# Optimization experiments

Measured on AMD Instinct MI355X. Metric: run time of the kernel, lower is better.

The kernel has to match this reference:

```python
import jax, jax.numpy as jnp
import numpy as np

BETA = 15.0  # soft-max temperature used by the common Erosion2d/Dilation2d (soft_max=True)
EPS = 1e-5


def _morph(x, w, dilation, kind):
    """Channel-wise soft morphological op over a KxK dilated window ('same' padding).
    erosion: -logsumexp(beta*(w - patch))/beta ; dilation: logsumexp(beta*(w + patch))/beta.
    """
    B, C, H, W = x.shape
    K = w.shape[-1]
    eff = K + (K - 1) * (dilation - 1)
    pb = (eff - 1) // 2
    pe = (eff - 1) - pb
    xp = jnp.pad(x, ((0, 0), (0, 0), (pb, pe), (pb, pe)))
    taps = [xp[:, :, i * dilation:i * dilation + H, j * dilation:j * dilation + W]
            for i in range(K) for j in range(K)]
    patches = jnp.stack(taps, axis=2)                      # (B, C, K*K, H, W)
    wf = w.reshape(C, K * K, 1, 1)                          # broadcast over B, H, W
    z = (wf - patches) if kind == 'erosion' else (wf + patches)
    out = jax.scipy.special.logsumexp(z * BETA, axis=2) / BETA  # (B, C, H, W)
    return -out if kind == 'erosion' else out


def _bn(x, gamma, beta):
    """BatchNorm2d in training mode: batch statistics over (B, H, W) per channel."""
    mean = jnp.mean(x, axis=(0, 2, 3), keepdims=True)
    var = jnp.var(x, axis=(0, 2, 3), keepdims=True)
    g = gamma.reshape(1, -1, 1, 1)
    b = beta.reshape(1, -1, 1, 1)
    return g * (x - mean) * jax.lax.rsqrt(var + EPS) + b


def setup_inputs() -> dict:
    key = jax.random.key(0)
    ks = jax.random.split(key, 5)
    B, C, H, W, K = 8, 64, 192, 192, 3
    x = jax.random.normal(ks[0], (B, C, H, W), jnp.float32)
    # morphology structuring elements (torch init is zeros; small randn for a nontrivial test)
    we = jax.random.normal(ks[1], (3, C, K, K), jnp.float32) * 0.1
    wd = jax.random.normal(ks[2], (3, C, K, K), jnp.float32) * 0.1
    # per-branch BN affine params (torch default: gamma=1, beta=0)
    bn_ge = jnp.ones((3, C), jnp.float32)
    bn_be = jnp.zeros((3, C), jnp.float32)
    bn_gd = jnp.ones((3, C), jnp.float32)
    bn_bd = jnp.zeros((3, C), jnp.float32)
    # 1x1 conv (3C -> 1, no bias): weight (1, 3C, 1, 1) stored flat as (3C,)
    conve_w = jax.random.normal(ks[3], (3 * C,), jnp.float32) * 0.05
    convd_w = jax.random.normal(ks[4], (3 * C,), jnp.float32) * 0.05
    g_e = jnp.ones((1,), jnp.float32)
    b_e = jnp.zeros((1,), jnp.float32)
    g_d = jnp.ones((1,), jnp.float32)
    b_d = jnp.zeros((1,), jnp.float32)
    return dict(x=x, we=we, wd=wd, bn_ge=bn_ge, bn_be=bn_be, bn_gd=bn_gd, bn_bd=bn_bd,
                conve_w=conve_w, convd_w=convd_w, g_e=g_e, b_e=b_e, g_d=g_d, b_d=b_d)


def reference(x, we, wd, bn_ge, bn_be, bn_gd, bn_bd, conve_w, convd_w, g_e, b_e, g_d, b_d):
    # three erosion branches (dilations 1,2,3), each followed by its own BN
    xe = jnp.concatenate([
        _bn(_morph(x, we[i], i + 1, 'erosion'), bn_ge[i], bn_be[i]) for i in range(3)
    ], axis=1)                                              # (B, 3C, H, W)
    xd = jnp.concatenate([
        _bn(_morph(x, wd[i], i + 1, 'dilation'), bn_gd[i], bn_bd[i]) for i in range(3)
    ], axis=1)
    # 1x1 conv to 1 channel + BN + ReLU
    ye = jnp.einsum('bchw,c->bhw', xe, conve_w)[:, None]    # (B, 1, H, W)
    ye = jax.nn.relu(_bn(ye, g_e, b_e))
    yd = jnp.einsum('bchw,c->bhw', xd, convd_w)[:, None]
    yd = jax.nn.relu(_bn(yd, g_d, b_d))
    return jnp.concatenate([ye, yd], axis=1)                # (B, 2, H, W)
```

## Files before the change

### kernel.cpp

```cpp
#include <hip/hip_runtime.h>


#define BETA 15.0f
#define MSHIFT 25.0f
#define INV_BETA (1.0f/15.0f)
#define LN2 0.6931471805599453f
#define EPSB 1e-5f
#define Hn 192
#define Wn 192
#define HWn (192*192)
#define N1 (8*192*192)
#define SFLOOR 1e-37f

#define STDH 70
#define STDW 70
#define STSTR 72
#define SNPAIR (STDH*35)

#define RDH 38
#define RSTR 40
#define RNPAIR (RDH*19)
#define RPITER 3

#define WS_SUM   0
#define WS_SQS   384
#define WS_SCAL  768
#define WS_WG    772
#define WS_YE    (772 + 3456)
#define WS_YD    (WS_YE + 294912)
#define WS_SLAB  (WS_YE + 2*294912)

__global__ void k_wexp(const float* __restrict__ we,
                       const float* __restrict__ wd,
                       float* __restrict__ ws) {
    int idx = blockIdx.x * 256 + threadIdx.x;
    if (idx < 772) ws[idx] = 0.f;
    if (idx >= 3456) return;
    int kb = idx / 576;
    int rem = idx - kb * 576;
    float w = (kb < 3) ? we[kb * 576 + rem] : wd[(kb - 3) * 576 + rem];
    ws[WS_WG + idx] = __expf(BETA * w);
}

template<int D, int H, int STR>
__device__ __forceinline__ void sweepT(const float* __restrict__ P,
                                       int py0, int px,
                                       const float* __restrict__ wgp,
                                       float* __restrict__ S) {
    float W[9];
#pragma unroll
    for (int k2 = 0; k2 < 9; ++k2) W[k2] = wgp[k2];
#pragma unroll
    for (int k = 0; k < H; ++k) S[k] = 0.f;
    const float* base = P + (py0 - D + 3) * STR + (px - D);
#pragma unroll
    for (int r = 0; r < H + 2 * D; ++r) {
        float va = base[r * STR];
        float vb = base[r * STR + D];
        float vc = base[r * STR + 2 * D];
#pragma unroll
        for (int i = 0; i < 3; ++i) {
            int k = r - i * D;
            if (k >= 0 && k < H) {
                S[k] = fmaf(W[i*3+0], va, S[k]);
                S[k] = fmaf(W[i*3+1], vb, S[k]);
                S[k] = fmaf(W[i*3+2], vc, S[k]);
            }
        }
    }
}

template<int D>
__device__ __forceinline__ void sweep2(const float* __restrict__ P,
                                       int py0, int tcol,
                                       const float* __restrict__ wgp,
                                       float* __restrict__ SA,
                                       float* __restrict__ SB) {
    float W[9];
#pragma unroll
    for (int k2 = 0; k2 < 9; ++k2) W[k2] = wgp[k2];
#pragma unroll
    for (int k = 0; k < 8; ++k) { SA[k] = 0.f; SB[k] = 0.f; }
    const int colbase = (D == 1) ? (2 * tcol + 2) : (2 * tcol);
#pragma unroll
    for (int r = 0; r < 8 + 2 * D; ++r) {
        const float2* row =
            (const float2*)(P + (py0 - D + 3 + r) * STSTR + colbase);
        float2 v0 = row[0], v1 = row[1];
        float ta0, ta1, ta2, tb0, tb1, tb2;
        if (D == 1) {
            ta0 = v0.x; ta1 = v0.y; ta2 = v1.x;
            tb0 = v0.y; tb1 = v1.x; tb2 = v1.y;
        } else {
            float2 v2 = row[2], v3 = row[3];
            if (D == 2) {
                ta0 = v0.y; ta1 = v1.y; ta2 = v2.y;
                tb0 = v1.x; tb1 = v2.x; tb2 = v3.x;
            } else {
                ta0 = v0.x; ta1 = v1.y; ta2 = v3.x;
                tb0 = v0.y; tb1 = v2.x; tb2 = v3.y;
            }
        }
#pragma unroll
        for (int i = 0; i < 3; ++i) {
            int k = r - i * D;
            if (k >= 0 && k < 8) {
                SA[k] = fmaf(W[i*3+0], ta0, SA[k]);
                SA[k] = fmaf(W[i*3+1], ta1, SA[k]);
                SA[k] = fmaf(W[i*3+2], ta2, SA[k]);
                SB[k] = fmaf(W[i*3+0], tb0, SB[k]);
                SB[k] = fmaf(W[i*3+1], tb1, SB[k]);
                SB[k] = fmaf(W[i*3+2], tb2, SB[k]);
            }
        }
    }
}

__device__ __forceinline__ void red2(float a, float b2, int lane, float* rs, float* rq) {
#pragma unroll
    for (int off = 32; off; off >>= 1) {
        a  += __shfl_down(a, off, 64);
        b2 += __shfl_down(b2, off, 64);
    }
    if (lane == 0) { *rs = a; *rq = b2; }
}

__global__ __launch_bounds__(256, 3) void k_stats(
    const float* __restrict__ x, const float* __restrict__ wg,
    float* __restrict__ sum, float* __restrict__ sqs) {
    __shared__ float EX[STDH * STSTR], EY[STDH * STSTR];
    __shared__ float redS[4][6], redQ[4][6];
    const int tid = threadIdx.x;
    const int p = blockIdx.y;
    const int c = p & 63;
    const int t = blockIdx.x;
    const int h0 = (t / 3) * 64, w0 = (t % 3) * 64;

    const float* xp = x + (size_t)p * HWn;
    {
        int r = tid / 35, pp = tid - r * 35;
        for (int l = tid; l < SNPAIR; l += 256) {
            int gh = h0 - 3 + r;
            int gw0 = w0 - 3 + 2 * pp;
            float va = 0.f, vb = 0.f;
            if ((unsigned)gh < (unsigned)Hn) {
                if ((unsigned)gw0 < (unsigned)Wn)       va = xp[gh * Wn + gw0];
                if ((unsigned)(gw0+1) < (unsigned)Wn)   vb = xp[gh * Wn + gw0 + 1];
            }
            float ba = BETA * va, bb = BETA * vb;
            *(float2*)&EX[r * STSTR + 2 * pp] =
                make_float2(__expf(-ba - MSHIFT), __expf(-bb - MSHIFT));
            *(float2*)&EY[r * STSTR + 2 * pp] =
                make_float2(__expf( ba - MSHIFT), __expf( bb - MSHIFT));
            r += 7; pp += 11;
            if (pp >= 35) { pp -= 35; ++r; }
        }
    }
    __syncthreads();

    const int tcol = tid & 31;
    const int py0 = (tid >> 5) * 8;
    const int lane = tid & 63, wv = tid >> 6;
    const float LI = LN2 * INV_BETA, MI = MSHIFT * INV_BETA;

#define DO_BR_STATS(D, SLOT, PL, AL, AM) { \
    float SA[8], SB[8]; \
    sweep2<D>(PL, py0, tcol, wg + (SLOT) * 576 + c * 9, SA, SB); \
    float sv = 0.f, qv = 0.f; \
    _Pragma("unroll") \
    for (int k = 0; k < 8; ++k) { \
        float ma = fmaf(__log2f(fmaxf(SA[k], SFLOOR)), AL, AM); \
        float mb = fmaf(__log2f(fmaxf(SB[k], SFLOOR)), AL, AM); \
        sv += ma + mb; qv = fmaf(ma, ma, fmaf(mb, mb, qv)); \
    } \
    red2(sv, qv, lane, &redS[wv][SLOT], &redQ[wv][SLOT]); }

    DO_BR_STATS(1, 0, EX, -LI, -MI)
    DO_BR_STATS(2, 1, EX, -LI, -MI)
    DO_BR_STATS(3, 2, EX, -LI, -MI)
    DO_BR_STATS(1, 3, EY,  LI,  MI)
    DO_BR_STATS(2, 4, EY,  LI,  MI)
    DO_BR_STATS(3, 5, EY,  LI,  MI)
#undef DO_BR_STATS

    __syncthreads();
    if (tid < 6)
        atomicAdd(&sum[tid * 64 + c],
                  redS[0][tid] + redS[1][tid] + redS[2][tid] + redS[3][tid]);
    else if (tid < 12) {
        int v = tid - 6;
        atomicAdd(&sqs[v * 64 + c],
                  redQ[0][v] + redQ[1][v] + redQ[2][v] + redQ[3][v]);
    }
}

__device__ __forceinline__ void alpha_fill(
    const float* __restrict__ sum, const float* __restrict__ sqs,
    const float* __restrict__ bn_ge, const float* __restrict__ bn_gd,
    const float* __restrict__ conve, const float* __restrict__ convd,
    float* __restrict__ al, int tid) {
    for (int l = tid; l < 384; l += 256) {
        int side_ = l / 192, ch = l - side_ * 192;
        float mean = sum[l] * (1.0f / N1);
        float var  = sqs[l] * (1.0f / N1) - mean * mean;
        float inv  = rsqrtf(fmaxf(var, 0.f) + EPSB);
        float g  = side_ ? bn_gd[ch] : bn_ge[ch];
        float cw = side_ ? convd[ch] : conve[ch];
        float sgn = side_ ? 1.f : -1.f;
        al[l] = sgn * cw * g * inv * INV_BETA * LN2;
    }
}

template<int NS>
__global__ __launch_bounds__(256, 4) void k_reduce(
    const float* __restrict__ x, const float* __restrict__ wg,
    const float* __restrict__ sum, const float* __restrict__ sqs,
    const float* __restrict__ bn_ge, const float* __restrict__ bn_gd,
    const float* __restrict__ conve, const float* __restrict__ convd,
    float* __restrict__ ye, float* __restrict__ yd,
    float* __restrict__ slab, float* __restrict__ scal) {
    constexpr int NC = 64 / NS;
    __shared__ float EX[RDH * RSTR], EY[RDH * RSTR];
    __shared__ float al[384];
    __shared__ float redA[4][4];
    const int tid = threadIdx.x;
    const int t = blockIdx.x;
    const int b = blockIdx.y;
    const int grp = blockIdx.z;
    const int c0 = grp * NC;
    const int tr = t / 6, tc = t - tr * 6;
    const int h0 = tr * 32, w0 = tc * 32;
    const int px = (tid & 31) + 3;
    const int py0 = (tid >> 5) * 4;
    const float* xb = x + (size_t)b * 64 * HWn;

    alpha_fill(sum, sqs, bn_ge, bn_gd, conve, convd, al, tid);

    float accE[4] = {0.f, 0.f, 0.f, 0.f}, accD[4] = {0.f, 0.f, 0.f, 0.f};
    float2 L[RPITER];

    {
        const float* xp = xb + (size_t)c0 * HWn;
        int r = tid / 19, pp = tid - r * 19;
#pragma unroll
        for (int i = 0; i < RPITER; ++i) {
            int l = tid + i * 256;
            float va = 0.f, vb = 0.f;
            if (l < RNPAIR) {
                int gh = h0 - 3 + r, gw0 = w0 - 3 + 2 * pp;
                if ((unsigned)gh < (unsigned)Hn) {
                    if ((unsigned)gw0 < (unsigned)Wn)     va = xp[gh * Wn + gw0];
                    if ((unsigned)(gw0+1) < (unsigned)Wn) vb = xp[gh * Wn + gw0 + 1];
                }
            }
            L[i] = make_float2(va, vb);
            r += 13; pp += 9;
            if (pp >= 19) { pp -= 19; ++r; }
        }
    }

    for (int ci = 0; ci < NC; ++ci) {
        __syncthreads();
        {
            int r = tid / 19, pp = tid - r * 19;
#pragma unroll
            for (int i = 0; i < RPITER; ++i) {
                int l = tid + i * 256;
                if (l < RNPAIR) {
                    float ba = BETA * L[i].x, bb = BETA * L[i].y;
                    *(float2*)&EX[r * RSTR + 2 * pp] =
                        make_float2(__expf(-ba - MSHIFT), __expf(-bb - MSHIFT));
                    *(float2*)&EY[r * RSTR + 2 * pp] =
                        make_float2(__expf( ba - MSHIFT), __expf( bb - MSHIFT));
                }
                r += 13; pp += 9;
                if (pp >= 19) { pp -= 19; ++r; }
            }
        }
        __syncthreads();
        if (ci < NC - 1) {
            const float* xp = xb + (size_t)(c0 + ci + 1) * HWn;
            int r = tid / 19, pp = tid - r * 19;
#pragma unroll
            for (int i = 0; i < RPITER; ++i) {
                int l = tid + i * 256;
                float va = 0.f, vb = 0.f;
                if (l < RNPAIR) {
                    int gh = h0 - 3 + r, gw0 = w0 - 3 + 2 * pp;
                    if ((unsigned)gh < (unsigned)Hn) {
                        if ((unsigned)gw0 < (unsigned)Wn)     va = xp[gh * Wn + gw0];
                        if ((unsigned)(gw0+1) < (unsigned)Wn) vb = xp[gh * Wn + gw0 + 1];
                    }
                }
                L[i] = make_float2(va, vb);
                r += 13; pp += 9;
                if (pp >= 19) { pp -= 19; ++r; }
            }
        }
        const int c = c0 + ci;
#define DO_BR_ACC(D, SIDE, BR, PL, ACC) { \
        float S[4]; \
        sweepT<D, 4, RSTR>(PL, py0, px, wg + ((SIDE) * 3 + (BR)) * 576 + c * 9, S); \
        const float a_ = al[(SIDE) * 192 + (BR) * 64 + c]; \
        _Pragma("unroll") \
        for (int k = 0; k < 4; ++k) \
            ACC[k] = fmaf(a_, __log2f(fmaxf(S[k], SFLOOR)), ACC[k]); }

        DO_BR_ACC(1, 0, 0, EX, accE)
        DO_BR_ACC(2, 0, 1, EX, accE)
        DO_BR_ACC(3, 0, 2, EX, accE)
        DO_BR_ACC(1, 1, 0, EY, accD)
        DO_BR_ACC(2, 1, 1, EY, accD)
        DO_BR_ACC(3, 1, 2, EY, accD)
#undef DO_BR_ACC
    }

    if constexpr (NS == 1) {
        const int oidx = b * HWn + (h0 + py0) * Wn + (w0 + px - 3);
#pragma unroll
        for (int k = 0; k < 4; ++k) {
            ye[oidx + k * Wn] = accE[k];
            yd[oidx + k * Wn] = accD[k];
        }
        float se = 0.f, qe = 0.f, sd = 0.f, qd = 0.f;
#pragma unroll
        for (int k = 0; k < 4; ++k) {
            se += accE[k]; qe = fmaf(accE[k], accE[k], qe);
            sd += accD[k]; qd = fmaf(accD[k], accD[k], qd);
        }
        const int lane = tid & 63, wv = tid >> 6;
        float v4[4] = {se, qe, sd, qd};
#pragma unroll
        for (int j = 0; j < 4; ++j) {
            float tv = v4[j];
#pragma unroll
            for (int off = 32; off; off >>= 1) tv += __shfl_down(tv, off, 64);
            if (lane == 0) redA[wv][j] = tv;
        }
        __syncthreads();
        if (tid < 4)
            atomicAdd(&scal[tid],
                      redA[0][tid] + redA[1][tid] + redA[2][tid] + redA[3][tid]);
    } else {
        float* pe = slab + ((size_t)grp * 8 + b) * HWn;
        float* pd = slab + ((size_t)(NS + grp) * 8 + b) * HWn;
        const int oidx = (h0 + py0) * Wn + (w0 + px - 3);
#pragma unroll
        for (int k = 0; k < 4; ++k) {
            pe[oidx + k * Wn] = accE[k];
            pd[oidx + k * Wn] = accD[k];
        }
    }
}

template<int NS>
__global__ __launch_bounds__(256) void k_fsum(
    const float* __restrict__ slab,
    float* __restrict__ ye, float* __restrict__ yd, float* __restrict__ scal) {
    int i = blockIdx.x * 256 + threadIdx.x;
    int b = i / HWn, rem = i - b * HWn;
    float e = 0.f, d = 0.f;
#pragma unroll
    for (int g = 0; g < NS; ++g) {
        e += slab[((size_t)g * 8 + b) * HWn + rem];
        d += slab[((size_t)(NS + g) * 8 + b) * HWn + rem];
    }
    ye[i] = e; yd[i] = d;
    float v[4] = {e, e * e, d, d * d};
    __shared__ float red[4][4];
    int lane = threadIdx.x & 63, wv = threadIdx.x >> 6;
#pragma unroll
    for (int k = 0; k < 4; ++k) {
        float tv = v[k];
#pragma unroll
        for (int off = 32; off; off >>= 1) tv += __shfl_down(tv, off, 64);
        if (lane == 0) red[wv][k] = tv;
    }
    __syncthreads();
    if (threadIdx.x < 4)
        atomicAdd(&scal[threadIdx.x],
                  red[0][threadIdx.x] + red[1][threadIdx.x] + red[2][threadIdx.x] + red[3][threadIdx.x]);
}

__global__ __launch_bounds__(256) void k_final(
    const float* __restrict__ ye, const float* __restrict__ yd,
    const float* __restrict__ scal,
    const float* __restrict__ g_e, const float* __restrict__ b_e,
    const float* __restrict__ g_d, const float* __restrict__ b_d,
    float* __restrict__ out) {
    int i = blockIdx.x * 256 + threadIdx.x;
    float me_ = scal[0] * (1.0f / N1);
    float ve  = scal[1] * (1.0f / N1) - me_ * me_;
    float ie  = rsqrtf(fmaxf(ve, 0.f) + EPSB);
    float md_ = scal[2] * (1.0f / N1);
    float vd  = scal[3] * (1.0f / N1) - md_ * md_;
    float idv = rsqrtf(fmaxf(vd, 0.f) + EPSB);
    float ge = g_e[0], be = b_e[0];
    float gd = g_d[0], bd = b_d[0];
    int b = i / HWn, rem = i - b * HWn;
    float oe = fmaxf(ge * (ye[i] - me_) * ie + be, 0.f);
    float od = fmaxf(gd * (yd[i] - md_) * idv + bd, 0.f);
    out[(size_t)(b * 2) * HWn + rem]     = oe;
    out[(size_t)(b * 2 + 1) * HWn + rem] = od;
}

extern "C" void kernel_launch(void* const* d_in, const int* in_sizes, int n_in,
                              void* d_out, int out_size, void* d_ws, size_t ws_size,
                              hipStream_t stream) {
    const float* x     = (const float*)d_in[0];
    const float* we    = (const float*)d_in[1];
    const float* wd    = (const float*)d_in[2];
    const float* bn_ge = (const float*)d_in[3];
    const float* bn_gd = (const float*)d_in[5];
    const float* conve = (const float*)d_in[7];
    const float* convd = (const float*)d_in[8];
    const float* g_e   = (const float*)d_in[9];
    const float* b_e   = (const float*)d_in[10];
    const float* g_d   = (const float*)d_in[11];
    const float* b_d   = (const float*)d_in[12];
    float* ws = (float*)d_ws;

    const size_t need4 = (size_t)(WS_SLAB + 4 * 2 * 294912) * sizeof(float);
    const size_t need2 = (size_t)(WS_SLAB + 2 * 2 * 294912) * sizeof(float);
    const int ns = (ws_size >= need4) ? 4 : (ws_size >= need2) ? 2 : 1;

    hipLaunchKernelGGL(k_wexp, dim3(14), dim3(256), 0, stream, we, wd, ws);
    hipLaunchKernelGGL(k_stats, dim3(9, 512), dim3(256), 0, stream,
                       x, ws + WS_WG, ws + WS_SUM, ws + WS_SQS);
    if (ns == 4) {
        hipLaunchKernelGGL((k_reduce<4>), dim3(36, 8, 4), dim3(256), 0, stream,
                           x, ws + WS_WG, ws + WS_SUM, ws + WS_SQS, bn_ge, bn_gd,
                           conve, convd, ws + WS_YE, ws + WS_YD, ws + WS_SLAB,
                           ws + WS_SCAL);
        hipLaunchKernelGGL((k_fsum<4>), dim3(1152), dim3(256), 0, stream,
                           ws + WS_SLAB, ws + WS_YE, ws + WS_YD, ws + WS_SCAL);
    } else if (ns == 2) {
        hipLaunchKernelGGL((k_reduce<2>), dim3(36, 8, 2), dim3(256), 0, stream,
                           x, ws + WS_WG, ws + WS_SUM, ws + WS_SQS, bn_ge, bn_gd,
                           conve, convd, ws + WS_YE, ws + WS_YD, ws + WS_SLAB,
                           ws + WS_SCAL);
        hipLaunchKernelGGL((k_fsum<2>), dim3(1152), dim3(256), 0, stream,
                           ws + WS_SLAB, ws + WS_YE, ws + WS_YD, ws + WS_SCAL);
    } else {
        hipLaunchKernelGGL((k_reduce<1>), dim3(36, 8, 1), dim3(256), 0, stream,
                           x, ws + WS_WG, ws + WS_SUM, ws + WS_SQS, bn_ge, bn_gd,
                           conve, convd, ws + WS_YE, ws + WS_YD, ws, ws + WS_SCAL);
    }
    hipLaunchKernelGGL(k_final, dim3(1152), dim3(256), 0, stream,
                       ws + WS_YE, ws + WS_YD, ws + WS_SCAL, g_e, b_e, g_d, b_d,
                       (float*)d_out);
}
```

Before: 282.0 us.

## Drop weight-exp kernel, replace stats atomics with partials, stop materializing ye/yd

```diff
diff --git a/kernel.cpp b/kernel.cpp
--- a/kernel.cpp
+++ b/kernel.cpp
@@ -13,7 +13,6 @@
 #define SFLOOR 1e-37f
 
 #define STDH 70
-#define STDW 70
 #define STSTR 72
 #define SNPAIR (STDH*35)
 
@@ -22,25 +21,11 @@
 #define RNPAIR (RDH*19)
 #define RPITER 3
 
-#define WS_SUM   0
-#define WS_SQS   384
-#define WS_SCAL  768
-#define WS_WG    772
-#define WS_YE    (772 + 3456)
-#define WS_YD    (WS_YE + 294912)
-#define WS_SLAB  (WS_YE + 2*294912)
-
-__global__ void k_wexp(const float* __restrict__ we,
-                       const float* __restrict__ wd,
-                       float* __restrict__ ws) {
-    int idx = blockIdx.x * 256 + threadIdx.x;
-    if (idx < 772) ws[idx] = 0.f;
-    if (idx >= 3456) return;
-    int kb = idx / 576;
-    int rem = idx - kb * 576;
-    float w = (kb < 3) ? we[kb * 576 + rem] : wd[(kb - 3) * 576 + rem];
-    ws[WS_WG + idx] = __expf(BETA * w);
-}
+#define WS_PART_S 0
+#define WS_PART_Q 27648
+#define WS_SCAL   55296
+#define WS_WG     55300
+#define WS_SLAB   58756
 
 template<int D, int H, int STR>
 __device__ __forceinline__ void sweepT(const float* __restrict__ P,
@@ -126,15 +111,29 @@
 }
 
 __global__ __launch_bounds__(256, 3) void k_stats(
-    const float* __restrict__ x, const float* __restrict__ wg,
-    float* __restrict__ sum, float* __restrict__ sqs) {
+    const float* __restrict__ x,
+    const float* __restrict__ we, const float* __restrict__ wd,
+    float* __restrict__ part_s, float* __restrict__ part_q,
+    float* __restrict__ wg, float* __restrict__ scal) {
     __shared__ float EX[STDH * STSTR], EY[STDH * STSTR];
+    __shared__ float wgl[54];
     __shared__ float redS[4][6], redQ[4][6];
     const int tid = threadIdx.x;
     const int p = blockIdx.y;
     const int c = p & 63;
+    const int b = p >> 6;
     const int t = blockIdx.x;
     const int h0 = (t / 3) * 64, w0 = (t % 3) * 64;
+
+    if (t == 0 && p == 0 && tid < 4) scal[tid] = 0.f;
+    if (tid < 54) {
+        int slot = tid / 9, k = tid - slot * 9;
+        const float* wsrc = (slot < 3) ? we : wd;
+        int br = (slot < 3) ? slot : slot - 3;
+        float v = __expf(BETA * wsrc[br * 576 + c * 9 + k]);
+        wgl[tid] = v;
+        if (t == 0) wg[slot * 576 + c * 9 + k] = v;
+    }
 
     const float* xp = x + (size_t)p * HWn;
     {
@@ -165,7 +164,7 @@
 
 #define DO_BR_STATS(D, SLOT, PL, AL, AM) { \
     float SA[8], SB[8]; \
-    sweep2<D>(PL, py0, tcol, wg + (SLOT) * 576 + c * 9, SA, SB); \
+    sweep2<D>(PL, py0, tcol, &wgl[(SLOT) * 9], SA, SB); \
     float sv = 0.f, qv = 0.f; \
     _Pragma("unroll") \
     for (int k = 0; k < 8; ++k) { \
@@ -185,44 +184,25 @@
 
     __syncthreads();
     if (tid < 6)
-        atomicAdd(&sum[tid * 64 + c],
-                  redS[0][tid] + redS[1][tid] + redS[2][tid] + redS[3][tid]);
+        part_s[(tid * 64 + c) * 72 + t * 8 + b] =
+            redS[0][tid] + redS[1][tid] + redS[2][tid] + redS[3][tid];
     else if (tid < 12) {
         int v = tid - 6;
-        atomicAdd(&sqs[v * 64 + c],
-                  redQ[0][v] + redQ[1][v] + redQ[2][v] + redQ[3][v]);
-    }
-}
-
-__device__ __forceinline__ void alpha_fill(
-    const float* __restrict__ sum, const float* __restrict__ sqs,
-    const float* __restrict__ bn_ge, const float* __restrict__ bn_gd,
-    const float* __restrict__ conve, const float* __restrict__ convd,
-    float* __restrict__ al, int tid) {
-    for (int l = tid; l < 384; l += 256) {
-        int side_ = l / 192, ch = l - side_ * 192;
-        float mean = sum[l] * (1.0f / N1);
-        float var  = sqs[l] * (1.0f / N1) - mean * mean;
-        float inv  = rsqrtf(fmaxf(var, 0.f) + EPSB);
-        float g  = side_ ? bn_gd[ch] : bn_ge[ch];
-        float cw = side_ ? convd[ch] : conve[ch];
-        float sgn = side_ ? 1.f : -1.f;
-        al[l] = sgn * cw * g * inv * INV_BETA * LN2;
+        part_q[(v * 64 + c) * 72 + t * 8 + b] =
+            redQ[0][v] + redQ[1][v] + redQ[2][v] + redQ[3][v];
     }
 }
 
 template<int NS>
 __global__ __launch_bounds__(256, 4) void k_reduce(
     const float* __restrict__ x, const float* __restrict__ wg,
-    const float* __restrict__ sum, const float* __restrict__ sqs,
+    const float* __restrict__ part_s, const float* __restrict__ part_q,
     const float* __restrict__ bn_ge, const float* __restrict__ bn_gd,
     const float* __restrict__ conve, const float* __restrict__ convd,
-    float* __restrict__ ye, float* __restrict__ yd,
-    float* __restrict__ slab, float* __restrict__ scal) {
+    float* __restrict__ slab) {
     constexpr int NC = 64 / NS;
     __shared__ float EX[RDH * RSTR], EY[RDH * RSTR];
     __shared__ float al[384];
-    __shared__ float redA[4][4];
     const int tid = threadIdx.x;
     const int t = blockIdx.x;
     const int b = blockIdx.y;
@@ -234,7 +214,23 @@
     const int py0 = (tid >> 5) * 4;
     const float* xb = x + (size_t)b * 64 * HWn;
 
-    alpha_fill(sum, sqs, bn_ge, bn_gd, conve, convd, al, tid);
+    for (int l = tid; l < 6 * NC; l += 256) {
+        int slot = l / NC, cl = l - slot * NC;
+        int ai = slot * 64 + c0 + cl;
+        const float* ps = part_s + (size_t)ai * 72;
+        const float* pq = part_q + (size_t)ai * 72;
+        float s = 0.f, q = 0.f;
+#pragma unroll
+        for (int j = 0; j < 72; ++j) { s += ps[j]; q += pq[j]; }
+        float mean = s * (1.0f / N1);
+        float var  = q * (1.0f / N1) - mean * mean;
+        float inv  = rsqrtf(fmaxf(var, 0.f) + EPSB);
+        int side_ = slot / 3, ch = ai - side_ * 192;
+        float g  = side_ ? bn_gd[ch] : bn_ge[ch];
+        float cw = side_ ? convd[ch] : conve[ch];
+        float sgn = side_ ? 1.f : -1.f;
+        al[ai] = sgn * cw * g * inv * INV_BETA * LN2;
+    }
 
     float accE[4] = {0.f, 0.f, 0.f, 0.f}, accD[4] = {0.f, 0.f, 0.f, 0.f};
     float2 L[RPITER];
@@ -315,57 +311,27 @@
 #undef DO_BR_ACC
     }
 
-    if constexpr (NS == 1) {
-        const int oidx = b * HWn + (h0 + py0) * Wn + (w0 + px - 3);
-#pragma unroll
-        for (int k = 0; k < 4; ++k) {
-            ye[oidx + k * Wn] = accE[k];
-            yd[oidx + k * Wn] = accD[k];
-        }
-        float se = 0.f, qe = 0.f, sd = 0.f, qd = 0.f;
-#pragma unroll
-        for (int k = 0; k < 4; ++k) {
-            se += accE[k]; qe = fmaf(accE[k], accE[k], qe);
-            sd += accD[k]; qd = fmaf(accD[k], accD[k], qd);
-        }
-        const int lane = tid & 63, wv = tid >> 6;
-        float v4[4] = {se, qe, sd, qd};
-#pragma unroll
-        for (int j = 0; j < 4; ++j) {
-            float tv = v4[j];
-#pragma unroll
-            for (int off = 32; off; off >>= 1) tv += __shfl_down(tv, off, 64);
-            if (lane == 0) redA[wv][j] = tv;
-        }
-        __syncthreads();
-        if (tid < 4)
-            atomicAdd(&scal[tid],
-                      redA[0][tid] + redA[1][tid] + redA[2][tid] + redA[3][tid]);
-    } else {
-        float* pe = slab + ((size_t)grp * 8 + b) * HWn;
-        float* pd = slab + ((size_t)(NS + grp) * 8 + b) * HWn;
-        const int oidx = (h0 + py0) * Wn + (w0 + px - 3);
-#pragma unroll
-        for (int k = 0; k < 4; ++k) {
-            pe[oidx + k * Wn] = accE[k];
-            pd[oidx + k * Wn] = accD[k];
-        }
+    float* pe = slab + ((size_t)(grp * 8 + b)) * HWn;
+    float* pd = slab + ((size_t)((NS + grp) * 8 + b)) * HWn;
+    const int oidx = (h0 + py0) * Wn + (w0 + px - 3);
+#pragma unroll
+    for (int k = 0; k < 4; ++k) {
+        pe[oidx + k * Wn] = accE[k];
+        pd[oidx + k * Wn] = accD[k];
     }
 }
 
 template<int NS>
 __global__ __launch_bounds__(256) void k_fsum(
-    const float* __restrict__ slab,
-    float* __restrict__ ye, float* __restrict__ yd, float* __restrict__ scal) {
+    const float* __restrict__ slab, float* __restrict__ scal) {
     int i = blockIdx.x * 256 + threadIdx.x;
     int b = i / HWn, rem = i - b * HWn;
     float e = 0.f, d = 0.f;
 #pragma unroll
     for (int g = 0; g < NS; ++g) {
-        e += slab[((size_t)g * 8 + b) * HWn + rem];
-        d += slab[((size_t)(NS + g) * 8 + b) * HWn + rem];
-    }
-    ye[i] = e; yd[i] = d;
+        e += slab[((size_t)(g * 8 + b)) * HWn + rem];
+        d += slab[((size_t)((NS + g) * 8 + b)) * HWn + rem];
+    }
     float v[4] = {e, e * e, d, d * d};
     __shared__ float red[4][4];
     int lane = threadIdx.x & 63, wv = threadIdx.x >> 6;
@@ -382,24 +348,28 @@
                   red[0][threadIdx.x] + red[1][threadIdx.x] + red[2][threadIdx.x] + red[3][threadIdx.x]);
 }
 
+template<int NS>
 __global__ __launch_bounds__(256) void k_final(
-    const float* __restrict__ ye, const float* __restrict__ yd,
-    const float* __restrict__ scal,
+    const float* __restrict__ slab, const float* __restrict__ scal,
     const float* __restrict__ g_e, const float* __restrict__ b_e,
     const float* __restrict__ g_d, const float* __restrict__ b_d,
     float* __restrict__ out) {
     int i = blockIdx.x * 256 + threadIdx.x;
+    int b = i / HWn, rem = i - b * HWn;
+    float e = 0.f, d = 0.f;
+#pragma unroll
+    for (int g = 0; g < NS; ++g) {
+        e += slab[((size_t)(g * 8 + b)) * HWn + rem];
+        d += slab[((size_t)((NS + g) * 8 + b)) * HWn + rem];
+    }
     float me_ = scal[0] * (1.0f / N1);
     float ve  = scal[1] * (1.0f / N1) - me_ * me_;
     float ie  = rsqrtf(fmaxf(ve, 0.f) + EPSB);
     float md_ = scal[2] * (1.0f / N1);
     float vd  = scal[3] * (1.0f / N1) - md_ * md_;
     float idv = rsqrtf(fmaxf(vd, 0.f) + EPSB);
-    float ge = g_e[0], be = b_e[0];
-    float gd = g_d[0], bd = b_d[0];
-    int b = i / HWn, rem = i - b * HWn;
-    float oe = fmaxf(ge * (ye[i] - me_) * ie + be, 0.f);
-    float od = fmaxf(gd * (yd[i] - md_) * idv + bd, 0.f);
+    float oe = fmaxf(g_e[0] * (e - me_) * ie + b_e[0], 0.f);
+    float od = fmaxf(g_d[0] * (d - md_) * idv + b_d[0], 0.f);
     out[(size_t)(b * 2) * HWn + rem]     = oe;
     out[(size_t)(b * 2 + 1) * HWn + rem] = od;
 }
@@ -420,33 +390,35 @@
     const float* b_d   = (const float*)d_in[12];
     float* ws = (float*)d_ws;
 
-    const size_t need4 = (size_t)(WS_SLAB + 4 * 2 * 294912) * sizeof(float);
-    const size_t need2 = (size_t)(WS_SLAB + 2 * 2 * 294912) * sizeof(float);
+    float* part_s = ws + WS_PART_S;
+    float* part_q = ws + WS_PART_Q;
+    float* scal   = ws + WS_SCAL;
+    float* wg     = ws + WS_WG;
+    float* slab   = ws + WS_SLAB;
+
+    const size_t need4 = (size_t)(WS_SLAB + 8 * 294912) * sizeof(float);
+    const size_t need2 = (size_t)(WS_SLAB + 4 * 294912) * sizeof(float);
     const int ns = (ws_size >= need4) ? 4 : (ws_size >= need2) ? 2 : 1;
 
-    hipLaunchKernelGGL(k_wexp, dim3(14), dim3(256), 0, stream, we, wd, ws);
     hipLaunchKernelGGL(k_stats, dim3(9, 512), dim3(256), 0, stream,
-                       x, ws + WS_WG, ws + WS_SUM, ws + WS_SQS);
+                       x, we, wd, part_s, part_q, wg, scal);
     if (ns == 4) {
         hipLaunchKernelGGL((k_reduce<4>), dim3(36, 8, 4), dim3(256), 0, stream,
-                           x, ws + WS_WG, ws + WS_SUM, ws + WS_SQS, bn_ge, bn_gd,
-                           conve, convd, ws + WS_YE, ws + WS_YD, ws + WS_SLAB,
-                           ws + WS_SCAL);
-        hipLaunchKernelGGL((k_fsum<4>), dim3(1152), dim3(256), 0, stream,
-                           ws + WS_SLAB, ws + WS_YE, ws + WS_YD, ws + WS_SCAL);
+                           x, wg, part_s, part_q, bn_ge, bn_gd, conve, convd, slab);
+        hipLaunchKernelGGL((k_fsum<4>), dim3(1152), dim3(256), 0, stream, slab, scal);
+        hipLaunchKernelGGL((k_final<4>), dim3(1152), dim3(256), 0, stream,
+                           slab, scal, g_e, b_e, g_d, b_d, (float*)d_out);
     } else if (ns == 2) {
         hipLaunchKernelGGL((k_reduce<2>), dim3(36, 8, 2), dim3(256), 0, stream,
-                           x, ws + WS_WG, ws + WS_SUM, ws + WS_SQS, bn_ge, bn_gd,
-                           conve, convd, ws + WS_YE, ws + WS_YD, ws + WS_SLAB,
-                           ws + WS_SCAL);
-        hipLaunchKernelGGL((k_fsum<2>), dim3(1152), dim3(256), 0, stream,
-                           ws + WS_SLAB, ws + WS_YE, ws + WS_YD, ws + WS_SCAL);
+                           x, wg, part_s, part_q, bn_ge, bn_gd, conve, convd, slab);
+        hipLaunchKernelGGL((k_fsum<2>), dim3(1152), dim3(256), 0, stream, slab, scal);
+        hipLaunchKernelGGL((k_final<2>), dim3(1152), dim3(256), 0, stream,
+                           slab, scal, g_e, b_e, g_d, b_d, (float*)d_out);
     } else {
         hipLaunchKernelGGL((k_reduce<1>), dim3(36, 8, 1), dim3(256), 0, stream,
-                           x, ws + WS_WG, ws + WS_SUM, ws + WS_SQS, bn_ge, bn_gd,
-                           conve, convd, ws + WS_YE, ws + WS_YD, ws, ws + WS_SCAL);
-    }
-    hipLaunchKernelGGL(k_final, dim3(1152), dim3(256), 0, stream,
-                       ws + WS_YE, ws + WS_YD, ws + WS_SCAL, g_e, b_e, g_d, b_d,
-                       (float*)d_out);
-}
+                           x, wg, part_s, part_q, bn_ge, bn_gd, conve, convd, slab);
+        hipLaunchKernelGGL((k_fsum<1>), dim3(1152), dim3(256), 0, stream, slab, scal);
+        hipLaunchKernelGGL((k_final<1>), dim3(1152), dim3(256), 0, stream,
+                           slab, scal, g_e, b_e, g_d, b_d, (float*)d_out);
+    }
+}
```

Measured after the change: 284.8 us. About the same (+1.0%).
